# Kernel tuning notes

Hardware: AMD Instinct MI355X
Metric: run time of the kernel (lower is better)

## Reference

```python
import jax, jax.numpy as jnp
import numpy as np

TEMPERATURE = 1.0
BIG = 1e30  # sentinel for masked min/max
NEG = -1e30  # masked logit


def _masked_log_softmax(x, m):
    # m: bool mask [B, N]; rows with no valid entries are handled by the caller
    return jax.nn.log_softmax(jnp.where(m, x, NEG), axis=-1)


def setup_inputs() -> dict:
    key = jax.random.key(0)
    k1, k2, k3 = jax.random.split(key, 3)
    B, N = 4096, 6000
    y_pred = jax.random.normal(k1, (B, N), dtype=jnp.float32)
    y_true = jax.random.normal(k2, (B, N), dtype=jnp.float32) * 0.05  # daily returns scale
    masks = jax.random.randint(k3, (B, N), 0, 2, dtype=jnp.int32)
    return {"y_pred": y_pred, "y_true": y_true, "masks": masks}


def reference(y_pred, y_true, masks):
    m = masks > 0  # [B, N] bool
    mf = m.astype(y_pred.dtype)
    n = mf.sum(-1)  # [B] number of valid stocks per day
    valid = n >= 2  # rows with <2 valid entries are skipped (contribute 0)

    # min-max normalize y_true over valid entries (label_smoothing == 0)
    t_min = jnp.min(jnp.where(m, y_true, BIG), axis=-1, keepdims=True)
    t_max = jnp.max(jnp.where(m, y_true, -BIG), axis=-1, keepdims=True)
    rng = t_max - t_min
    true_norm = jnp.where(rng > 0, (y_true - t_min) / (rng + 1e-12), y_true)

    logp_pred = _masked_log_softmax(y_pred / TEMPERATURE, m)
    logp_true = _masked_log_softmax(true_norm / TEMPERATURE, m)
    p_true = jnp.exp(logp_true)

    # F.kl_div(pred_prob.log(), true_prob, reduction='batchmean') on a 1-D
    # vector of length n divides the summed KL by n.
    kl_elem = jnp.where(m, p_true * (logp_true - logp_pred), 0.0)
    kl = kl_elem.sum(-1) / jnp.maximum(n, 1.0)  # [B]

    batch_size = y_pred.shape[0]
    return jnp.sum(jnp.where(valid, kl, 0.0)) / batch_size
```

## Files before the change

kernel.cpp:

```cpp
#include <hip/hip_runtime.h>
#include <math.h>

#define NCOL  6000
#define NV    1500
#define BLOCK 512
#define NWAVE 8
#define EPT   3

__device__ __forceinline__ float wave_max_f(float v) {
    #pragma unroll
    for (int off = 32; off > 0; off >>= 1) v = fmaxf(v, __shfl_xor(v, off, 64));
    return v;
}
__device__ __forceinline__ float wave_min_f(float v) {
    #pragma unroll
    for (int off = 32; off > 0; off >>= 1) v = fminf(v, __shfl_xor(v, off, 64));
    return v;
}
__device__ __forceinline__ int wave_sum_i(int v) {
    #pragma unroll
    for (int off = 32; off > 0; off >>= 1) v += __shfl_xor(v, off, 64);
    return v;
}
__device__ __forceinline__ double wave_sum_d(double v) {
    #pragma unroll
    for (int off = 32; off > 0; off >>= 1) v += __shfl_xor(v, off, 64);
    return v;
}

__global__ __launch_bounds__(BLOCK, 4) void row_kl_kernel(
    const float* __restrict__ yp, const float* __restrict__ yt,
    const int* __restrict__ mk, float* __restrict__ rowkl)
{
    __shared__ float  swf[3][NWAVE];
    __shared__ int    swi[NWAVE];
    __shared__ double swd[3][NWAVE];

    const int row  = blockIdx.x;
    const int tid  = threadIdx.x;
    const int lane = tid & 63;
    const int wid  = tid >> 6;

    const float4* yp4 = reinterpret_cast<const float4*>(yp) + (size_t)row * NV;
    const float4* yt4 = reinterpret_cast<const float4*>(yt) + (size_t)row * NV;
    const int4*   mk4 = reinterpret_cast<const int4*>(mk) + (size_t)row * NV;

    const int v2 = tid + 2 * BLOCK;
    const int vc2 = (v2 < NV) ? v2 : 0;
    float4 xp[EPT], xt[EPT];
    int4   mm[EPT];
    xp[0] = yp4[tid];
    xp[1] = yp4[tid + BLOCK];
    xp[2] = yp4[vc2];
    xt[0] = yt4[tid];
    xt[1] = yt4[tid + BLOCK];
    xt[2] = yt4[vc2];
    mm[0] = mk4[tid];
    mm[1] = mk4[tid + BLOCK];
    mm[2] = mk4[vc2];
    if (v2 >= NV) { mm[2].x = 0; mm[2].y = 0; mm[2].z = 0; mm[2].w = 0; }

    float maxp = -1e30f, tmin = 1e30f, tmax = -1e30f;
    int cnt = 0;
    #pragma unroll
    for (int j = 0; j < EPT; ++j) {
        {
            bool m = mm[j].x > 0;
            float x = m ? xp[j].x : -1e30f;
            float t = m ? xt[j].x : -1e30f;
            tmin = fminf(tmin, m ? xt[j].x : 1e30f);
            xp[j].x = x; xt[j].x = t;
            maxp = fmaxf(maxp, x); tmax = fmaxf(tmax, t); cnt += m;
        }
        {
            bool m = mm[j].y > 0;
            float x = m ? xp[j].y : -1e30f;
            float t = m ? xt[j].y : -1e30f;
            tmin = fminf(tmin, m ? xt[j].y : 1e30f);
            xp[j].y = x; xt[j].y = t;
            maxp = fmaxf(maxp, x); tmax = fmaxf(tmax, t); cnt += m;
        }
        {
            bool m = mm[j].z > 0;
            float x = m ? xp[j].z : -1e30f;
            float t = m ? xt[j].z : -1e30f;
            tmin = fminf(tmin, m ? xt[j].z : 1e30f);
            xp[j].z = x; xt[j].z = t;
            maxp = fmaxf(maxp, x); tmax = fmaxf(tmax, t); cnt += m;
        }
        {
            bool m = mm[j].w > 0;
            float x = m ? xp[j].w : -1e30f;
            float t = m ? xt[j].w : -1e30f;
            tmin = fminf(tmin, m ? xt[j].w : 1e30f);
            xp[j].w = x; xt[j].w = t;
            maxp = fmaxf(maxp, x); tmax = fmaxf(tmax, t); cnt += m;
        }
    }

    maxp = wave_max_f(maxp);
    tmin = wave_min_f(tmin);
    tmax = wave_max_f(tmax);
    cnt  = wave_sum_i(cnt);
    if (lane == 0) { swf[0][wid] = maxp; swf[1][wid] = tmin; swf[2][wid] = tmax; swi[wid] = cnt; }
    __syncthreads();
    maxp = -1e30f; tmin = 1e30f; tmax = -1e30f; cnt = 0;
    #pragma unroll
    for (int j = 0; j < NWAVE; ++j) {
        maxp = fmaxf(maxp, swf[0][j]);
        tmin = fminf(tmin, swf[1][j]);
        tmax = fmaxf(tmax, swf[2][j]);
        cnt += swi[j];
    }

    const float rng   = tmax - tmin;
    const bool scaled = rng > 0.0f;
    const float inv_s = 1.0f / (rng + 1e-12f);
    const float maxz  = scaled ? rng * inv_s : tmax;

    double Zp = 0.0, S1 = 0.0, S2 = 0.0;
    #pragma unroll
    for (int j = 0; j < EPT; ++j) {
        #pragma unroll
        for (int c = 0; c < 4; ++c) {
            float x = (c == 0) ? xp[j].x : (c == 1) ? xp[j].y : (c == 2) ? xp[j].z : xp[j].w;
            float t = (c == 0) ? xt[j].x : (c == 1) ? xt[j].y : (c == 2) ? xt[j].z : xt[j].w;
            float ep = __expf(x - maxp);
            float z  = scaled ? (t - tmin) * inv_s : t;
            z = fmaxf(z, -1e30f);
            float e1 = __expf(z - maxz);
            Zp += (double)ep;
            S1 += (double)e1;
            S2 += (double)e1 * (double)(z - x);
        }
    }
    Zp = wave_sum_d(Zp);
    S1 = wave_sum_d(S1);
    S2 = wave_sum_d(S2);
    if (lane == 0) { swd[0][wid] = Zp; swd[1][wid] = S1; swd[2][wid] = S2; }
    __syncthreads();
    if (tid == 0) {
        double zp = 0.0, s1 = 0.0, s2 = 0.0;
        #pragma unroll
        for (int j = 0; j < NWAVE; ++j) { zp += swd[0][j]; s1 += swd[1][j]; s2 += swd[2][j]; }
        float val = 0.0f;
        if (cnt >= 2) {
            double kl = s2 / s1 + ((double)maxp + log(zp) - (double)maxz - log(s1));
            double v  = kl / (double)cnt;
            if (isfinite(v)) val = (float)v;
        }
        rowkl[row] = val;
    }
}

__global__ __launch_bounds__(256) void final_reduce_kernel(
    const float* __restrict__ rowkl, float* __restrict__ out, int nrows)
{
    __shared__ double swd[4];
    const int tid  = threadIdx.x;
    const int lane = tid & 63;
    const int wid  = tid >> 6;
    double acc = 0.0;
    for (int i = tid; i < nrows; i += 256) acc += (double)rowkl[i];
    acc = wave_sum_d(acc);
    if (lane == 0) swd[wid] = acc;
    __syncthreads();
    if (tid == 0) {
        double tot = 0.0;
        #pragma unroll
        for (int j = 0; j < 4; ++j) tot += swd[j];
        out[0] = (float)(tot / (double)nrows);
    }
}

extern "C" void kernel_launch(void* const* d_in, const int* in_sizes, int n_in,
                              void* d_out, int out_size, void* d_ws, size_t ws_size,
                              hipStream_t stream) {
    const float* y_pred = (const float*)d_in[0];
    const float* y_true = (const float*)d_in[1];
    const int*   masks  = (const int*)d_in[2];
    float* out = (float*)d_out;
    float* rowkl = (float*)d_ws;

    const int B = in_sizes[0] / NCOL;

    row_kl_kernel<<<B, BLOCK, 0, stream>>>(y_pred, y_true, masks, rowkl);
    final_reduce_kernel<<<1, 256, 0, stream>>>(rowkl, out, B);
}
```

Before: 56.83 us.

## Process eight rows per block with double-buffered register prefetch of next row

Each block now handles eight consecutive rows instead of one. It keeps two register payloads and issues the loads for the next row before reducing the current one. The aim is to hide global-memory latency inside each block and cut launch and block-scheduling overhead. The cost is a much smaller grid, 512 blocks, which may not saturate bandwidth as well. Holding two payloads under a 4-blocks-per-CU launch bound also roughly doubles live registers, which risks spills.

```diff
diff --git a/kernel.cpp b/kernel.cpp
--- a/kernel.cpp
+++ b/kernel.cpp
@@ -5,7 +5,13 @@
 #define NV    1500
 #define BLOCK 512
 #define NWAVE 8
-#define EPT   3
+#define RPB   8
+
+typedef struct {
+    float4 xp0, xp1, xp2;
+    float4 xt0, xt1, xt2;
+    int4   mm0, mm1, mm2;
+} Pay;
 
 __device__ __forceinline__ float wave_max_f(float v) {
     #pragma unroll
@@ -28,75 +34,52 @@
     return v;
 }
 
-__global__ __launch_bounds__(BLOCK, 4) void row_kl_kernel(
-    const float* __restrict__ yp, const float* __restrict__ yt,
-    const int* __restrict__ mk, float* __restrict__ rowkl)
-{
-    __shared__ float  swf[3][NWAVE];
-    __shared__ int    swi[NWAVE];
-    __shared__ double swd[3][NWAVE];
-
-    const int row  = blockIdx.x;
-    const int tid  = threadIdx.x;
-    const int lane = tid & 63;
-    const int wid  = tid >> 6;
-
-    const float4* yp4 = reinterpret_cast<const float4*>(yp) + (size_t)row * NV;
-    const float4* yt4 = reinterpret_cast<const float4*>(yt) + (size_t)row * NV;
-    const int4*   mk4 = reinterpret_cast<const int4*>(mk) + (size_t)row * NV;
-
-    const int v2 = tid + 2 * BLOCK;
-    const int vc2 = (v2 < NV) ? v2 : 0;
-    float4 xp[EPT], xt[EPT];
-    int4   mm[EPT];
-    xp[0] = yp4[tid];
-    xp[1] = yp4[tid + BLOCK];
-    xp[2] = yp4[vc2];
-    xt[0] = yt4[tid];
-    xt[1] = yt4[tid + BLOCK];
-    xt[2] = yt4[vc2];
-    mm[0] = mk4[tid];
-    mm[1] = mk4[tid + BLOCK];
-    mm[2] = mk4[vc2];
-    if (v2 >= NV) { mm[2].x = 0; mm[2].y = 0; mm[2].z = 0; mm[2].w = 0; }
+__device__ __forceinline__ void issue_row(
+    const float4* __restrict__ yp4, const float4* __restrict__ yt4,
+    const int4* __restrict__ mk4, size_t rbase, int tid, int vc2, Pay& P)
+{
+    const float4* p = yp4 + rbase;
+    const float4* t = yt4 + rbase;
+    const int4*   m = mk4 + rbase;
+    P.xp0 = p[tid]; P.xp1 = p[tid + BLOCK]; P.xp2 = p[vc2];
+    P.xt0 = t[tid]; P.xt1 = t[tid + BLOCK]; P.xt2 = t[vc2];
+    P.mm0 = m[tid]; P.mm1 = m[tid + BLOCK]; P.mm2 = m[vc2];
+}
+
+#define DO_MASK(MM, XP, XT, C) do {                                   \
+    bool  m_ = (MM).C > 0;                                            \
+    float x_ = m_ ? (XP).C : -1e30f;                                  \
+    float t_ = m_ ? (XT).C : -1e30f;                                  \
+    tmin = fminf(tmin, m_ ? (XT).C : 1e30f);                          \
+    (XP).C = x_; (XT).C = t_;                                         \
+    maxp = fmaxf(maxp, x_); tmax = fmaxf(tmax, t_); cnt += m_;        \
+} while (0)
+
+#define DO_KL(XP, XT, C) do {                                         \
+    float x_ = (XP).C, t_ = (XT).C;                                   \
+    float ep_ = __expf(x_ - maxp);                                    \
+    float z_  = scaled ? (t_ - tmin) * inv_s : t_;                    \
+    z_ = fmaxf(z_, -1e30f);                                           \
+    float e1_ = __expf(z_ - maxz);                                    \
+    Zp += (double)ep_; S1 += (double)e1_;                             \
+    S2 += (double)e1_ * (double)(z_ - x_);                            \
+} while (0)
+
+__device__ __forceinline__ void process_row(
+    Pay P, int v2, int tid, int lane, int wid,
+    float (*swf)[NWAVE], int* swi, double (*swd)[NWAVE],
+    float* __restrict__ rowkl, int row)
+{
+    if (v2 >= NV) { P.mm2.x = 0; P.mm2.y = 0; P.mm2.z = 0; P.mm2.w = 0; }
 
     float maxp = -1e30f, tmin = 1e30f, tmax = -1e30f;
     int cnt = 0;
-    #pragma unroll
-    for (int j = 0; j < EPT; ++j) {
-        {
-            bool m = mm[j].x > 0;
-            float x = m ? xp[j].x : -1e30f;
-            float t = m ? xt[j].x : -1e30f;
-            tmin = fminf(tmin, m ? xt[j].x : 1e30f);
-            xp[j].x = x; xt[j].x = t;
-            maxp = fmaxf(maxp, x); tmax = fmaxf(tmax, t); cnt += m;
-        }
-        {
-            bool m = mm[j].y > 0;
-            float x = m ? xp[j].y : -1e30f;
-            float t = m ? xt[j].y : -1e30f;
-            tmin = fminf(tmin, m ? xt[j].y : 1e30f);
-            xp[j].y = x; xt[j].y = t;
-            maxp = fmaxf(maxp, x); tmax = fmaxf(tmax, t); cnt += m;
-        }
-        {
-            bool m = mm[j].z > 0;
-            float x = m ? xp[j].z : -1e30f;
-            float t = m ? xt[j].z : -1e30f;
-            tmin = fminf(tmin, m ? xt[j].z : 1e30f);
-            xp[j].z = x; xt[j].z = t;
-            maxp = fmaxf(maxp, x); tmax = fmaxf(tmax, t); cnt += m;
-        }
-        {
-            bool m = mm[j].w > 0;
-            float x = m ? xp[j].w : -1e30f;
-            float t = m ? xt[j].w : -1e30f;
-            tmin = fminf(tmin, m ? xt[j].w : 1e30f);
-            xp[j].w = x; xt[j].w = t;
-            maxp = fmaxf(maxp, x); tmax = fmaxf(tmax, t); cnt += m;
-        }
-    }
+    DO_MASK(P.mm0, P.xp0, P.xt0, x); DO_MASK(P.mm0, P.xp0, P.xt0, y);
+    DO_MASK(P.mm0, P.xp0, P.xt0, z); DO_MASK(P.mm0, P.xp0, P.xt0, w);
+    DO_MASK(P.mm1, P.xp1, P.xt1, x); DO_MASK(P.mm1, P.xp1, P.xt1, y);
+    DO_MASK(P.mm1, P.xp1, P.xt1, z); DO_MASK(P.mm1, P.xp1, P.xt1, w);
+    DO_MASK(P.mm2, P.xp2, P.xt2, x); DO_MASK(P.mm2, P.xp2, P.xt2, y);
+    DO_MASK(P.mm2, P.xp2, P.xt2, z); DO_MASK(P.mm2, P.xp2, P.xt2, w);
 
     maxp = wave_max_f(maxp);
     tmin = wave_min_f(tmin);
@@ -119,21 +102,13 @@
     const float maxz  = scaled ? rng * inv_s : tmax;
 
     double Zp = 0.0, S1 = 0.0, S2 = 0.0;
-    #pragma unroll
-    for (int j = 0; j < EPT; ++j) {
-        #pragma unroll
-        for (int c = 0; c < 4; ++c) {
-            float x = (c == 0) ? xp[j].x : (c == 1) ? xp[j].y : (c == 2) ? xp[j].z : xp[j].w;
-            float t = (c == 0) ? xt[j].x : (c == 1) ? xt[j].y : (c == 2) ? xt[j].z : xt[j].w;
-            float ep = __expf(x - maxp);
-            float z  = scaled ? (t - tmin) * inv_s : t;
-            z = fmaxf(z, -1e30f);
-            float e1 = __expf(z - maxz);
-            Zp += (double)ep;
-            S1 += (double)e1;
-            S2 += (double)e1 * (double)(z - x);
-        }
-    }
+    DO_KL(P.xp0, P.xt0, x); DO_KL(P.xp0, P.xt0, y);
+    DO_KL(P.xp0, P.xt0, z); DO_KL(P.xp0, P.xt0, w);
+    DO_KL(P.xp1, P.xt1, x); DO_KL(P.xp1, P.xt1, y);
+    DO_KL(P.xp1, P.xt1, z); DO_KL(P.xp1, P.xt1, w);
+    DO_KL(P.xp2, P.xt2, x); DO_KL(P.xp2, P.xt2, y);
+    DO_KL(P.xp2, P.xt2, z); DO_KL(P.xp2, P.xt2, w);
+
     Zp = wave_sum_d(Zp);
     S1 = wave_sum_d(S1);
     S2 = wave_sum_d(S2);
@@ -153,6 +128,43 @@
     }
 }
 
+__global__ __launch_bounds__(BLOCK, 4) void row_kl_kernel(
+    const float* __restrict__ yp, const float* __restrict__ yt,
+    const int* __restrict__ mk, float* __restrict__ rowkl)
+{
+    __shared__ float  swf[3][NWAVE];
+    __shared__ int    swi[NWAVE];
+    __shared__ double swd[3][NWAVE];
+
+    const int tid  = threadIdx.x;
+    const int lane = tid & 63;
+    const int wid  = tid >> 6;
+    const int v2   = tid + 2 * BLOCK;
+    const int vc2  = (v2 < NV) ? v2 : 0;
+
+    const float4* yp4 = reinterpret_cast<const float4*>(yp);
+    const float4* yt4 = reinterpret_cast<const float4*>(yt);
+    const int4*   mk4 = reinterpret_cast<const int4*>(mk);
+
+    const int row0 = blockIdx.x * RPB;
+
+    Pay A, B;
+    issue_row(yp4, yt4, mk4, (size_t)row0 * NV, tid, vc2, A);
+    __builtin_amdgcn_sched_barrier(0);
+
+    #pragma unroll 1
+    for (int i = 0; i < RPB; i += 2) {
+        issue_row(yp4, yt4, mk4, (size_t)(row0 + i + 1) * NV, tid, vc2, B);
+        __builtin_amdgcn_sched_barrier(0);
+        process_row(A, v2, tid, lane, wid, swf, swi, swd, rowkl, row0 + i);
+
+        if (i + 2 < RPB)
+            issue_row(yp4, yt4, mk4, (size_t)(row0 + i + 2) * NV, tid, vc2, A);
+        __builtin_amdgcn_sched_barrier(0);
+        process_row(B, v2, tid, lane, wid, swf, swi, swd, rowkl, row0 + i + 1);
+    }
+}
+
 __global__ __launch_bounds__(256) void final_reduce_kernel(
     const float* __restrict__ rowkl, float* __restrict__ out, int nrows)
 {
@@ -184,6 +196,6 @@
 
     const int B = in_sizes[0] / NCOL;
 
-    row_kl_kernel<<<B, BLOCK, 0, stream>>>(y_pred, y_true, masks, rowkl);
+    row_kl_kernel<<<B / RPB, BLOCK, 0, stream>>>(y_pred, y_true, masks, rowkl);
     final_reduce_kernel<<<1, 256, 0, stream>>>(rowkl, out, B);
 }
```

Result: slower. 99.86 us (+75.7%).
